# Optimization experiments

Measured on AMD Instinct MI355X. Metric: run time of the kernel, lower is better.

## Reference

```python
import jax, jax.numpy as jnp
import numpy as np

N = 256        # nagents
HID = 256      # hid_size
OBS = 128      # obs_size
GAT_HID = 128  # gat_hid_size
H1 = 4         # gat_num_heads (first processor)
H2 = 1         # gat_num_heads_out (second processor)
NACT = 10      # single action head
NEG = 0.2      # leaky relu negative slope


def _lin(k, fan_in, fan_out, s=0.05):
    kw, kb = jax.random.split(k)
    return (jax.random.normal(kw, (fan_in, fan_out), jnp.float32) * s,
            jax.random.normal(kb, (fan_out,), jnp.float32) * s)


def setup_inputs() -> dict:
    key = jax.random.key(0)
    ks = jax.random.split(key, 32)
    p = {}
    p['obs'] = jax.random.normal(ks[0], (1, N, OBS), jnp.float32)
    p['hidden_state'] = jax.random.normal(ks[1], (N, HID), jnp.float32)
    p['cell_state'] = jax.random.normal(ks[2], (N, HID), jnp.float32)
    p['w_obs'], p['b_obs'] = _lin(ks[3], OBS, HID)
    p['w_ih'], p['b_ih'] = _lin(ks[4], HID, 4 * HID)   # LSTMCell input->gates (i,f,g,o)
    p['w_hh'], p['b_hh'] = _lin(ks[5], HID, 4 * HID)
    p['w_me'], p['b_me'] = _lin(ks[6], HID, HID)        # message encoder
    p['w_md'], p['b_md'] = _lin(ks[7], HID, HID)        # message decoder
    # sub_scheduler_mlp1: 2*HID -> HID//2 -> HID//8 -> 2
    p['s1_w1'], p['s1_b1'] = _lin(ks[8], 2 * HID, HID // 2)
    p['s1_w2'], p['s1_b2'] = _lin(ks[9], HID // 2, HID // 8)
    p['s1_w3'], p['s1_b3'] = _lin(ks[10], HID // 8, 2)
    # sub_scheduler_mlp2 (learn_second_graph)
    p['s2_w1'], p['s2_b1'] = _lin(ks[11], 2 * HID, HID // 2)
    p['s2_w2'], p['s2_b2'] = _lin(ks[12], HID // 2, HID // 8)
    p['s2_w3'], p['s2_b3'] = _lin(ks[13], HID // 8, 2)
    # GAT1: HID -> H1*GAT_HID (concat heads)
    p['g1_w'] = jax.random.normal(ks[14], (HID, H1 * GAT_HID), jnp.float32) * 0.05
    p['g1_ai'] = jax.random.normal(ks[15], (H1, GAT_HID), jnp.float32) * 0.05
    p['g1_aj'] = jax.random.normal(ks[16], (H1, GAT_HID), jnp.float32) * 0.05
    p['g1_b'] = jax.random.normal(ks[17], (H1 * GAT_HID,), jnp.float32) * 0.05
    # GAT2: H1*GAT_HID -> HID (average over heads)
    p['g2_w'] = jax.random.normal(ks[18], (H1 * GAT_HID, H2 * HID), jnp.float32) * 0.05
    p['g2_ai'] = jax.random.normal(ks[19], (H2, HID), jnp.float32) * 0.05
    p['g2_aj'] = jax.random.normal(ks[20], (H2, HID), jnp.float32) * 0.05
    p['g2_b'] = jax.random.normal(ks[21], (HID,), jnp.float32) * 0.05
    p['w_v'], p['b_v'] = _lin(ks[22], 2 * HID, 1)
    p['w_a'], p['b_a'] = _lin(ks[23], 2 * HID, NACT)
    return p


def _sub_scheduler(h, w1, b1, w2, b2, w3, b3, mask, key):
    # pairwise concat: pair[i,j] = [h_i, h_j]  -> [n, n, 2*hid]
    n, d = h.shape
    pair = jnp.concatenate([jnp.broadcast_to(h[:, None, :], (n, n, d)),
                            jnp.broadcast_to(h[None, :, :], (n, n, d))], axis=-1)
    z = jax.nn.relu(pair @ w1 + b1)
    z = jax.nn.relu(z @ w2 + b2)
    logits = z @ w3 + b3                                # [n, n, 2]
    # gumbel-softmax (tau=1, hard=True, straight-through)
    u = jax.random.uniform(key, logits.shape, minval=1e-10, maxval=1.0)
    gumbel = -jnp.log(-jnp.log(u))
    y = jax.nn.softmax(logits + gumbel, axis=-1)
    y_hard = jax.nn.one_hot(jnp.argmax(y, axis=-1), 2, dtype=y.dtype)
    y = y_hard + y - jax.lax.stop_gradient(y)
    adj = y[..., 1] * mask * mask.T                     # mask [n,1]
    return adj


def _gat(x, adj, W, ai, aj, b, average):
    # dense-adjacency multi-head GAT, self_loop_type=1 (force self loops)
    n = x.shape[0]
    heads, of = ai.shape
    h = (x @ W).reshape(n, heads, of)                   # [n, heads, out]
    eye = jnp.eye(n, dtype=x.dtype)
    adj = adj * (1.0 - eye) + eye
    ci = jnp.einsum('nhf,hf->nh', h, ai)
    cj = jnp.einsum('nhf,hf->nh', h, aj)
    e = jax.nn.leaky_relu(ci[:, None, :] + cj[None, :, :], NEG)   # [n, n, heads]
    att = jnp.where(adj[:, :, None] > 0, e, jnp.float32(-9e15))
    att = jax.nn.softmax(att, axis=1)
    att = att * adj[:, :, None]
    out = jnp.einsum('ijh,jhf->ihf', att, h)            # aggregate over neighbors j
    out = out.mean(axis=1) if average else out.reshape(n, heads * of)
    return out + b


def reference(obs, hidden_state, cell_state, w_obs, b_obs, w_ih, b_ih, w_hh, b_hh,
              w_me, b_me, w_md, b_md,
              s1_w1, s1_b1, s1_w2, s1_b2, s1_w3, s1_b3,
              s2_w1, s2_b1, s2_w2, s2_b2, s2_w3, s2_b3,
              g1_w, g1_ai, g1_aj, g1_b, g2_w, g2_ai, g2_aj, g2_b,
              w_v, b_v, w_a, b_a):
    x = (obs @ w_obs + b_obs)[0]                        # [n, hid]
    # LSTMCell, torch gate order (i, f, g, o)
    gates = x @ w_ih + b_ih + hidden_state @ w_hh + b_hh
    i, f, g, o = jnp.split(gates, 4, axis=-1)
    c_new = jax.nn.sigmoid(f) * cell_state + jax.nn.sigmoid(i) * jnp.tanh(g)
    h_new = jax.nn.sigmoid(o) * jnp.tanh(c_new)
    mask = jnp.ones((N, 1), jnp.float32)                # all agents alive
    comm = (h_new @ w_me + b_me) * mask
    comm_ori = comm
    adj1 = _sub_scheduler(comm, s1_w1, s1_b1, s1_w2, s1_b2, s1_w3, s1_b3,
                          mask, jax.random.key(1))
    comm = jax.nn.elu(_gat(comm, adj1, g1_w, g1_ai, g1_aj, g1_b, average=False))
    adj2 = _sub_scheduler(comm_ori, s2_w1, s2_b1, s2_w2, s2_b2, s2_w3, s2_b3,
                          mask, jax.random.key(2))
    comm = _gat(comm, adj2, g2_w, g2_ai, g2_aj, g2_b, average=True)
    comm = (comm * mask) @ w_md + b_md
    value = jnp.concatenate([h_new, comm], axis=-1) @ w_v + b_v      # [n, 1]
    hc = jnp.concatenate([h_new.reshape(1, N, HID), comm.reshape(1, N, HID)], axis=-1)
    action_out = jax.nn.log_softmax(hc @ w_a + b_a, axis=-1)         # [1, n, nact]
    return action_out, value, h_new, c_new
```

## Files before the change

### kernel.cpp

```cpp
#include <hip/hip_runtime.h>
#include <stdint.h>
#include <math.h>

#define NA 256

typedef __attribute__((ext_vector_type(4))) float f32x4;
typedef __attribute__((ext_vector_type(8))) short bfrag;
typedef __attribute__((ext_vector_type(4))) float cfrag;

__device__ __forceinline__ uint32_t rotl32_(uint32_t v, int d) {
    return (v << d) | (v >> (32 - d));
}

__device__ uint32_t jax_random_bits(uint32_t key_lo, uint32_t flat) {
    uint32_t a, b;
    bool first;
    if (flat < 65536u) { a = flat; b = flat + 65536u; first = true; }
    else               { a = flat - 65536u; b = flat; first = false; }
    uint32_t ks0 = 0u, ks1 = key_lo, ks2 = 0u ^ key_lo ^ 0x1BD11BDAu;
    uint32_t x0 = a + ks0, x1 = b + ks1;
    const int r0[4] = {13, 15, 26, 6};
    const int r1[4] = {17, 29, 16, 24};
#define TF_R4(RS) { for (int rr = 0; rr < 4; ++rr) { x0 += x1; x1 = rotl32_(x1, RS[rr]); x1 ^= x0; } }
    TF_R4(r0); x0 += ks1; x1 += ks2 + 1u;
    TF_R4(r1); x0 += ks2; x1 += ks0 + 2u;
    TF_R4(r0); x0 += ks0; x1 += ks1 + 3u;
    TF_R4(r1); x0 += ks1; x1 += ks2 + 4u;
    TF_R4(r0); x0 += ks2; x1 += ks0 + 5u;
#undef TF_R4
    return first ? x0 : x1;
}

__device__ float jax_gumbel(uint32_t key_lo, uint32_t flat) {
    uint32_t bits = jax_random_bits(key_lo, flat);
    uint32_t v = (bits >> 9) | 0x3F800000u;
    float u = __uint_as_float(v) - 1.0f;
    u = u + 1e-10f;
    u = fmaxf(1e-10f, u);
    return -logf(-logf(u));
}

__device__ __forceinline__ uint32_t f2bf(float f) {
    uint32_t u = __float_as_uint(f);
    return (u + 0x7FFFu + ((u >> 16) & 1u)) >> 16;
}

__global__ __launch_bounds__(256) void k_lstm(
        const float* __restrict__ obs, const float* __restrict__ hs,
        const float* __restrict__ cs,
        const float* __restrict__ w_obs, const float* __restrict__ b_obs,
        const float* __restrict__ w_ih, const float* __restrict__ b_ih,
        const float* __restrict__ w_hh, const float* __restrict__ b_hh,
        float* __restrict__ h_out, float* __restrict__ c_out) {
    __shared__ float o_l[8][128];
    __shared__ float h_l[8][256];
    __shared__ float x_l[8][256];
    __shared__ float red[8192];
    int r0 = blockIdx.x * 8, c0 = blockIdx.y * 32, t = threadIdx.x;
    ((f32x4*)o_l)[t] = ((const f32x4*)(obs + r0 * 128))[t];
    ((f32x4*)h_l)[t] = ((const f32x4*)(hs + r0 * 256))[t];
    ((f32x4*)h_l)[t + 256] = ((const f32x4*)(hs + r0 * 256))[t + 256];
    __syncthreads();
    {
        int ks = t >> 6, q = t & 63;
        f32x4 acc[8];
#pragma unroll
        for (int r = 0; r < 8; ++r) acc[r] = (f32x4){0.f, 0.f, 0.f, 0.f};
#pragma unroll
        for (int k = ks * 32; k < ks * 32 + 32; ++k) {
            f32x4 w = *(const f32x4*)(w_obs + k * 256 + q * 4);
#pragma unroll
            for (int r = 0; r < 8; ++r) {
                float xv = o_l[r][k];
                acc[r].x += xv * w.x; acc[r].y += xv * w.y;
                acc[r].z += xv * w.z; acc[r].w += xv * w.w;
            }
        }
#pragma unroll
        for (int r = 0; r < 8; ++r)
            *(f32x4*)&red[(ks * 8 + r) * 256 + q * 4] = acc[r];
    }
    __syncthreads();
    {
#pragma unroll
        for (int rep = 0; rep < 8; ++rep) {
            int o = t + rep * 256;
            int r = o >> 8, c = o & 255;
            float s = b_obs[c];
#pragma unroll
            for (int k2 = 0; k2 < 4; ++k2) s += red[(k2 * 8 + r) * 256 + c];
            x_l[r][c] = s;
        }
    }
    __syncthreads();
    {
        int ks = t >> 5, cg = t & 31;
        int g = cg >> 3, qd = cg & 7;
        int col = g * 256 + c0 + qd * 4;
        const float* W = (ks < 4) ? w_ih : w_hh;
        const float* xl = (ks < 4) ? &x_l[0][0] : &h_l[0][0];
        int kb = (ks & 3) * 64;
        f32x4 acc[8];
#pragma unroll
        for (int r = 0; r < 8; ++r) acc[r] = (f32x4){0.f, 0.f, 0.f, 0.f};
#pragma unroll
        for (int kk = 0; kk < 64; ++kk) {
            int k = kb + kk;
            f32x4 w = *(const f32x4*)(W + k * 1024 + col);
#pragma unroll
            for (int r = 0; r < 8; ++r) {
                float xv = xl[r * 256 + k];
                acc[r].x += xv * w.x; acc[r].y += xv * w.y;
                acc[r].z += xv * w.z; acc[r].w += xv * w.w;
            }
        }
        __syncthreads();
#pragma unroll
        for (int r = 0; r < 8; ++r)
            *(f32x4*)&red[(ks * 8 + r) * 128 + cg * 4] = acc[r];
    }
    __syncthreads();
    {
        int r = t >> 5, hc = t & 31;
        int gc = c0 + hc;
        float gate[4];
#pragma unroll
        for (int g = 0; g < 4; ++g) {
            float s = b_ih[g * 256 + gc] + b_hh[g * 256 + gc];
#pragma unroll
            for (int ks = 0; ks < 8; ++ks) s += red[(ks * 8 + r) * 128 + g * 32 + hc];
            gate[g] = s;
        }
        float ig = 1.f / (1.f + expf(-gate[0]));
        float fg = 1.f / (1.f + expf(-gate[1]));
        float gg = tanhf(gate[2]);
        float og = 1.f / (1.f + expf(-gate[3]));
        float cn = fg * cs[(r0 + r) * 256 + gc] + ig * gg;
        float hn = og * tanhf(cn);
        h_out[(r0 + r) * 256 + gc] = hn;
        c_out[(r0 + r) * 256 + gc] = cn;
    }
}

template<int K>
__device__ __forceinline__ void gemm_core(const float* __restrict__ X, int xs, int r0,
                                          const float* __restrict__ W, int ws,
                                          const float* __restrict__ bias,
                                          float* __restrict__ Y, int ys, int t,
                                          float* xr, float* red) {
    constexpr int KQ = K / 4;
#pragma unroll
    for (int q = t; q < 2 * K; q += 256) {
        int r = q / KQ, c = q % KQ;
        ((f32x4*)xr)[r * KQ + c] = ((const f32x4*)(X + (r0 + r) * xs))[c];
    }
    __syncthreads();
    constexpr int KP = K / 16;
    int qd = t & 15, ks = t >> 4;
    f32x4 acc[8];
#pragma unroll
    for (int r = 0; r < 8; ++r) acc[r] = (f32x4){0.f, 0.f, 0.f, 0.f};
#pragma unroll
    for (int k = ks * KP; k < ks * KP + KP; ++k) {
        f32x4 w = *(const f32x4*)(W + k * ws + qd * 4);
#pragma unroll
        for (int r = 0; r < 8; ++r) {
            float xv = xr[r * K + k];
            acc[r].x += xv * w.x; acc[r].y += xv * w.y;
            acc[r].z += xv * w.z; acc[r].w += xv * w.w;
        }
    }
#pragma unroll
    for (int r = 0; r < 8; ++r)
        *(f32x4*)&red[(ks * 8 + r) * 64 + qd * 4] = acc[r];
    __syncthreads();
#pragma unroll
    for (int rep = 0; rep < 2; ++rep) {
        int o = t + rep * 256;
        int r = o >> 6, c = o & 63;
        float s = bias ? bias[c] : 0.f;
#pragma unroll
        for (int ks2 = 0; ks2 < 16; ++ks2) s += red[(ks2 * 8 + r) * 64 + c];
        Y[(r0 + r) * ys + c] = s;
    }
}

template<int K>
__global__ __launch_bounds__(256) void k_gemm(const float* __restrict__ X, int xs,
                                              const float* __restrict__ W, int ws,
                                              const float* __restrict__ bias,
                                              float* __restrict__ Y, int ys) {
    __shared__ float xr[8 * K];
    __shared__ float red[16 * 8 * 64];
    int cb = blockIdx.y * 64;
    gemm_core<K>(X, xs, blockIdx.x * 8, W + cb, ws, bias ? bias + cb : nullptr,
                 Y + cb, ys, threadIdx.x, xr, red);
}

__global__ __launch_bounds__(256) void k_mgemm(const float* __restrict__ comm,
        const float* __restrict__ g1_w,
        const float* __restrict__ s1w1, const float* __restrict__ s1b1,
        const float* __restrict__ s2w1, const float* __restrict__ s2b1,
        float* __restrict__ h1, float* __restrict__ A1, float* __restrict__ B1,
        float* __restrict__ A2, float* __restrict__ B2) {
    __shared__ float xr[8 * 256];
    __shared__ float red[16 * 8 * 64];
    int y = blockIdx.y;
    const float* W; int ws; const float* bias; float* Y; int ys;
    if (y < 8) {
        W = g1_w + y * 64; ws = 512; bias = nullptr; Y = h1 + y * 64; ys = 512;
    } else {
        int idx = y - 8;
        int sel = idx >> 2, part = (idx >> 1) & 1, half = idx & 1;
        W = (sel ? s2w1 : s1w1) + part * (256 * 128) + half * 64; ws = 128;
        bias = part ? nullptr : ((sel ? s2b1 : s1b1) + half * 64);
        float* tgt = sel ? (part ? B2 : A2) : (part ? B1 : A1);
        Y = tgt + half * 64; ys = 128;
    }
    gemm_core<256>(comm, 256, blockIdx.x * 8, W, ws, bias, Y, ys, threadIdx.x, xr, red);
}

__global__ __launch_bounds__(256) void k_sched(
        const float* __restrict__ A1, const float* __restrict__ B1,
        const float* __restrict__ s1w2, const float* __restrict__ s1b2,
        const float* __restrict__ s1w3, const float* __restrict__ s1b3,
        const float* __restrict__ A2, const float* __restrict__ B2,
        const float* __restrict__ s2w2, const float* __restrict__ s2b2,
        const float* __restrict__ s2w3, const float* __restrict__ s2b3,
        float* __restrict__ adj1, float* __restrict__ adj2) {
    __shared__ __align__(16) char z1z2[65536];
    __shared__ __align__(16) char w2l[8192];
    __shared__ float a_l[128];
    __shared__ float b2_l[32], w3_l[64], b3_l[2];
    int i = blockIdx.x, t = threadIdx.x, s = blockIdx.y;
    const float* A  = s ? A2 : A1;
    const float* B  = s ? B2 : B1;
    const float* w2 = s ? s2w2 : s1w2;
    const float* b2 = s ? s2b2 : s1b2;
    const float* w3 = s ? s2w3 : s1w3;
    const float* b3 = s ? s2b3 : s1b3;
    float* adj = s ? adj2 : adj1;
    uint32_t key_lo = (uint32_t)(s + 1);

    if (t < 32) ((f32x4*)a_l)[t] = ((const f32x4*)(A + i * 128))[t];
    if (t < 32) b2_l[t] = b2[t];
    if (t < 64) w3_l[t] = w3[t];
    if (t < 2)  b3_l[t] = b3[t];
    {
        int c = t & 31, kq = t >> 5;
        uint32_t* dst = (uint32_t*)w2l;
#pragma unroll
        for (int e = 0; e < 8; ++e) {
            int k = kq * 16 + e * 2;
            uint32_t word = f2bf(w2[k * 32 + c]) | (f2bf(w2[(k + 1) * 32 + c]) << 16);
            int byte = (c * 256 + k * 2) ^ ((c & 7) << 4);
            dst[byte >> 2] = word;
        }
    }
    __syncthreads();
#pragma unroll
    for (int rep = 0; rep < 4; ++rep) {
        int j = (t >> 2) + rep * 64;
        int kq = t & 3;
        const f32x4* bp = (const f32x4*)(B + j * 128 + kq * 32);
        uint32_t words[16];
#pragma unroll
        for (int q = 0; q < 8; ++q) {
            f32x4 bv = bp[q];
            int k = kq * 32 + q * 4;
            float z0 = fmaxf(a_l[k] + bv.x, 0.f);
            float z1v = fmaxf(a_l[k + 1] + bv.y, 0.f);
            float z2v = fmaxf(a_l[k + 2] + bv.z, 0.f);
            float z3v = fmaxf(a_l[k + 3] + bv.w, 0.f);
            words[q * 2]     = f2bf(z0) | (f2bf(z1v) << 16);
            words[q * 2 + 1] = f2bf(z2v) | (f2bf(z3v) << 16);
        }
#pragma unroll
        for (int w4 = 0; w4 < 4; ++w4) {
            int byte = (j * 256 + kq * 64 + w4 * 16) ^ ((j & 7) << 4);
            *(uint4*)(z1z2 + byte) = make_uint4(words[w4 * 4], words[w4 * 4 + 1],
                                                words[w4 * 4 + 2], words[w4 * 4 + 3]);
        }
    }
    __syncthreads();
    int w = t >> 6, l = t & 63;
    bfrag bf[2][4];
#pragma unroll
    for (int ct = 0; ct < 2; ++ct)
#pragma unroll
        for (int ks = 0; ks < 4; ++ks) {
            int col = ct * 16 + (l & 15);
            int k = ks * 32 + (l >> 4) * 8;
            int byte = (col * 256 + k * 2) ^ ((col & 7) << 4);
            bf[ct][ks] = *(bfrag*)(w2l + byte);
        }
    cfrag acc[4][2];
    cfrag zz = {0.f, 0.f, 0.f, 0.f};
#pragma unroll
    for (int rt = 0; rt < 4; ++rt) { acc[rt][0] = zz; acc[rt][1] = zz; }
#pragma unroll
    for (int rt = 0; rt < 4; ++rt) {
        int j = (w * 4 + rt) * 16 + (l & 15);
#pragma unroll
        for (int ks = 0; ks < 4; ++ks) {
            int byte = (j * 256 + (ks * 32 + (l >> 4) * 8) * 2) ^ ((j & 7) << 4);
            bfrag af = *(bfrag*)(z1z2 + byte);
            acc[rt][0] = __builtin_amdgcn_mfma_f32_16x16x32_bf16(af, bf[0][ks], acc[rt][0], 0, 0, 0);
            acc[rt][1] = __builtin_amdgcn_mfma_f32_16x16x32_bf16(af, bf[1][ks], acc[rt][1], 0, 0, 0);
        }
    }
    __syncthreads();
    float* z2 = (float*)z1z2;
#pragma unroll
    for (int rt = 0; rt < 4; ++rt)
#pragma unroll
        for (int ct = 0; ct < 2; ++ct)
#pragma unroll
            for (int r = 0; r < 4; ++r) {
                int j = (w * 4 + rt) * 16 + (l >> 4) * 4 + r;
                int c = ct * 16 + (l & 15);
                z2[j * 36 + c] = acc[rt][ct][r];
            }
    __syncthreads();
    {
        int j = t;
        float p0 = 0.f, p1 = 0.f;
#pragma unroll
        for (int c = 0; c < 32; ++c) {
            float zv = fmaxf(z2[j * 36 + c] + b2_l[c], 0.f);
            p0 += zv * w3_l[2 * c];
            p1 += zv * w3_l[2 * c + 1];
        }
        float l0 = p0 + b3_l[0], l1 = p1 + b3_l[1];
        uint32_t flat = (uint32_t)(i * 256 + j) * 2u;
        float g0 = jax_gumbel(key_lo, flat);
        float g1 = jax_gumbel(key_lo, flat + 1u);
        adj[i * 256 + j] = (l1 + g1 > l0 + g0) ? 1.0f : 0.0f;
    }
}

__global__ void k_attc(const float* __restrict__ H, const float* __restrict__ ai,
                       const float* __restrict__ aj, float* __restrict__ ci,
                       float* __restrict__ cj, int heads, int F) {
    int n = blockIdx.x, lane = threadIdx.x;
    for (int h = 0; h < heads; ++h) {
        float pi = 0.f, pj = 0.f;
        for (int f = lane; f < F; f += 64) {
            float v = H[n * heads * F + h * F + f];
            pi += v * ai[h * F + f];
            pj += v * aj[h * F + f];
        }
        for (int off = 32; off; off >>= 1) {
            pi += __shfl_xor(pi, off);
            pj += __shfl_xor(pj, off);
        }
        if (lane == 0) { ci[n * heads + h] = pi; cj[n * heads + h] = pj; }
    }
}

__global__ __launch_bounds__(256) void k_gat1(const float* __restrict__ H,
        const float* __restrict__ adj, const float* __restrict__ ci,
        const float* __restrict__ cj, const float* __restrict__ bias,
        float* __restrict__ out) {
    __shared__ float att[2][4][256];
    __shared__ float red[4][2][256];
    int i0 = blockIdx.x * 2, cb = blockIdx.y * 256, t = threadIdx.x;
#pragma unroll
    for (int r = 0; r < 2; ++r) {
        int i = i0 + r;
        float adjv = (t == i) ? 1.f : adj[i * 256 + t];
#pragma unroll
        for (int h = 0; h < 4; ++h) {
            float e = ci[i * 4 + h] + cj[t * 4 + h];
            e = e >= 0.f ? e : 0.2f * e;
            att[r][h][t] = adjv > 0.f ? e : -INFINITY;
        }
    }
    __syncthreads();
    {
        int wv = t >> 6, lane = t & 63;
        for (int p = wv; p < 8; p += 4) {
            int r = p >> 2, h = p & 3;
            float* ar = att[r][h];
            float m = -INFINITY;
            for (int j = lane; j < 256; j += 64) m = fmaxf(m, ar[j]);
            for (int off = 32; off; off >>= 1) m = fmaxf(m, __shfl_xor(m, off));
            float vals[4], sm = 0.f;
#pragma unroll
            for (int q = 0; q < 4; ++q) {
                float v = expf(ar[lane + 64 * q] - m);
                vals[q] = v; sm += v;
            }
            for (int off = 32; off; off >>= 1) sm += __shfl_xor(sm, off);
            float inv = 1.f / sm;
#pragma unroll
            for (int q = 0; q < 4; ++q) ar[lane + 64 * q] = vals[q] * inv;
        }
    }
    __syncthreads();
    {
        int q = t & 63, js = t >> 6;
        int c = cb + q * 4;
        int h = c >> 7;
        f32x4 a0 = {0.f, 0.f, 0.f, 0.f}, a1 = a0;
        const float* ar0 = att[0][h];
        const float* ar1 = att[1][h];
#pragma unroll
        for (int j = js * 64; j < js * 64 + 64; ++j) {
            f32x4 hv = *(const f32x4*)(H + j * 512 + c);
            float v0 = ar0[j], v1 = ar1[j];
            a0.x += v0 * hv.x; a0.y += v0 * hv.y; a0.z += v0 * hv.z; a0.w += v0 * hv.w;
            a1.x += v1 * hv.x; a1.y += v1 * hv.y; a1.z += v1 * hv.z; a1.w += v1 * hv.w;
        }
        *(f32x4*)&red[js][0][q * 4] = a0;
        *(f32x4*)&red[js][1][q * 4] = a1;
    }
    __syncthreads();
#pragma unroll
    for (int rep = 0; rep < 2; ++rep) {
        int o = t + rep * 256;
        int r = o >> 8, c = o & 255;
        float s = red[0][r][c] + red[1][r][c] + red[2][r][c] + red[3][r][c] + bias[cb + c];
        out[(i0 + r) * 512 + cb + c] = s > 0.f ? s : expm1f(s);
    }
}

__global__ __launch_bounds__(256) void k_final(const float* __restrict__ H,
        const float* __restrict__ adj, const float* __restrict__ ci,
        const float* __restrict__ cj, const float* __restrict__ g2_b,
        const float* __restrict__ w_md, const float* __restrict__ b_md,
        const float* __restrict__ h_new,
        const float* __restrict__ w_v, const float* __restrict__ b_v,
        const float* __restrict__ w_a, const float* __restrict__ b_a,
        float* __restrict__ value, float* __restrict__ action) {
    __shared__ float att[256];
    __shared__ float buf[4][256];
    __shared__ float out2[256];
    __shared__ float comm3[256];
    __shared__ float hrow[256];
    __shared__ float hred[4][16];
    __shared__ float vred[4];
    int i = blockIdx.x, t = threadIdx.x;
    hrow[t] = h_new[i * 256 + t];
    {
        float adjv = (t == i) ? 1.f : adj[i * 256 + t];
        float e = ci[i] + cj[t];
        e = e >= 0.f ? e : 0.2f * e;
        att[t] = adjv > 0.f ? e : -INFINITY;
    }
    __syncthreads();
    {
        int lane = t & 63;
        float m = -INFINITY;
        for (int j = lane; j < 256; j += 64) m = fmaxf(m, att[j]);
        for (int off = 32; off; off >>= 1) m = fmaxf(m, __shfl_xor(m, off));
        float sm = 0.f;
        for (int j = lane; j < 256; j += 64) sm += expf(att[j] - m);
        for (int off = 32; off; off >>= 1) sm += __shfl_xor(sm, off);
        float inv = 1.f / sm;
        float myval = expf(att[t] - m) * inv;
        __syncthreads();
        att[t] = myval;
    }
    __syncthreads();
    {
        int q = t & 63, js = t >> 6;
        f32x4 acc = {0.f, 0.f, 0.f, 0.f};
#pragma unroll
        for (int j = js * 64; j < js * 64 + 64; ++j) {
            f32x4 hv = *(const f32x4*)(H + j * 256 + q * 4);
            float av = att[j];
            acc.x += av * hv.x; acc.y += av * hv.y; acc.z += av * hv.z; acc.w += av * hv.w;
        }
        *(f32x4*)&buf[js][q * 4] = acc;
    }
    __syncthreads();
    out2[t] = buf[0][t] + buf[1][t] + buf[2][t] + buf[3][t] + g2_b[t];
    __syncthreads();
    {
        int q = t & 63, ks = t >> 6;
        f32x4 acc = {0.f, 0.f, 0.f, 0.f};
#pragma unroll
        for (int k = ks * 64; k < ks * 64 + 64; ++k) {
            f32x4 wv = *(const f32x4*)(w_md + k * 256 + q * 4);
            float xv = out2[k];
            acc.x += xv * wv.x; acc.y += xv * wv.y; acc.z += xv * wv.z; acc.w += xv * wv.w;
        }
        *(f32x4*)&buf[ks][q * 4] = acc;
    }
    __syncthreads();
    comm3[t] = buf[0][t] + buf[1][t] + buf[2][t] + buf[3][t] + b_md[t];
    __syncthreads();
    int w = t >> 6, l = t & 63;
    {
        float p = hrow[t] * w_v[t] + comm3[t] * w_v[256 + t];
        for (int off = 32; off; off >>= 1) p += __shfl_xor(p, off);
        if (l == 0) vred[w] = p;
    }
    {
        int o = l & 15;
        int kseg = w * 4 + (l >> 4);
        float acc = 0.f;
        if (o < 10) {
#pragma unroll
            for (int kk = 0; kk < 32; ++kk) {
                int k = kseg * 32 + kk;
                float x = (kseg < 8) ? hrow[k] : comm3[k - 256];
                acc += x * w_a[k * 10 + o];
            }
        }
        acc += __shfl_xor(acc, 16);
        acc += __shfl_xor(acc, 32);
        if (l < 16) hred[w][l] = acc;
    }
    __syncthreads();
    if (t < 16) {
        int o = t;
        float logit = (o < 10)
            ? hred[0][o] + hred[1][o] + hred[2][o] + hred[3][o] + b_a[o]
            : -INFINITY;
        float m = logit;
        for (int off = 8; off; off >>= 1) m = fmaxf(m, __shfl_xor(m, off));
        float ex = (o < 10) ? expf(logit - m) : 0.f;
        float sm = ex;
        for (int off = 8; off; off >>= 1) sm += __shfl_xor(sm, off);
        if (o < 10) action[i * 10 + o] = logit - m - logf(sm);
        if (o == 0) value[i] = vred[0] + vred[1] + vred[2] + vred[3] + b_v[0];
    }
}

extern "C" void kernel_launch(void* const* d_in, const int* in_sizes, int n_in,
                              void* d_out, int out_size, void* d_ws, size_t ws_size,
                              hipStream_t stream) {
    const float* obs   = (const float*)d_in[0];
    const float* hs    = (const float*)d_in[1];
    const float* cs    = (const float*)d_in[2];
    const float* w_obs = (const float*)d_in[3];
    const float* b_obs = (const float*)d_in[4];
    const float* w_ih  = (const float*)d_in[5];
    const float* b_ih  = (const float*)d_in[6];
    const float* w_hh  = (const float*)d_in[7];
    const float* b_hh  = (const float*)d_in[8];
    const float* w_me  = (const float*)d_in[9];
    const float* b_me  = (const float*)d_in[10];
    const float* w_md  = (const float*)d_in[11];
    const float* b_md  = (const float*)d_in[12];
    const float* s1_w1 = (const float*)d_in[13];
    const float* s1_b1 = (const float*)d_in[14];
    const float* s1_w2 = (const float*)d_in[15];
    const float* s1_b2 = (const float*)d_in[16];
    const float* s1_w3 = (const float*)d_in[17];
    const float* s1_b3 = (const float*)d_in[18];
    const float* s2_w1 = (const float*)d_in[19];
    const float* s2_b1 = (const float*)d_in[20];
    const float* s2_w2 = (const float*)d_in[21];
    const float* s2_b2 = (const float*)d_in[22];
    const float* s2_w3 = (const float*)d_in[23];
    const float* s2_b3 = (const float*)d_in[24];
    const float* g1_w  = (const float*)d_in[25];
    const float* g1_ai = (const float*)d_in[26];
    const float* g1_aj = (const float*)d_in[27];
    const float* g1_b  = (const float*)d_in[28];
    const float* g2_w  = (const float*)d_in[29];
    const float* g2_ai = (const float*)d_in[30];
    const float* g2_aj = (const float*)d_in[31];
    const float* g2_b  = (const float*)d_in[32];
    const float* w_v   = (const float*)d_in[33];
    const float* b_v   = (const float*)d_in[34];
    const float* w_a   = (const float*)d_in[35];
    const float* b_a   = (const float*)d_in[36];

    float* out = (float*)d_out;
    float* action = out;
    float* value  = out + 2560;
    float* h_new  = out + 2816;
    float* c_new  = out + 68352;

    float* ws = (float*)d_ws;
    float* comm  = ws;
    float* A1    = ws + 65536;
    float* B1    = ws + 98304;
    float* A2    = ws + 131072;
    float* B2    = ws + 163840;
    float* adj1  = ws + 196608;
    float* adj2  = ws + 262144;
    float* h1    = ws + 327680;
    float* ci1   = ws + 458752;
    float* cj1   = ws + 459776;
    float* comm2 = ws + 460800;
    float* h2    = ws + 591872;
    float* ci2   = ws + 657408;
    float* cj2   = ws + 657664;

    k_lstm<<<dim3(32, 8), 256, 0, stream>>>(obs, hs, cs, w_obs, b_obs,
                                            w_ih, b_ih, w_hh, b_hh, h_new, c_new);
    k_gemm<256><<<dim3(32, 4), 256, 0, stream>>>(h_new, 256, w_me, 256, b_me, comm, 256);
    k_mgemm<<<dim3(32, 16), 256, 0, stream>>>(comm, g1_w, s1_w1, s1_b1, s2_w1, s2_b1,
                                              h1, A1, B1, A2, B2);
    k_sched<<<dim3(256, 2), 256, 0, stream>>>(A1, B1, s1_w2, s1_b2, s1_w3, s1_b3,
                                              A2, B2, s2_w2, s2_b2, s2_w3, s2_b3,
                                              adj1, adj2);
    k_attc<<<NA, 64, 0, stream>>>(h1, g1_ai, g1_aj, ci1, cj1, 4, 128);
    k_gat1<<<dim3(128, 2), 256, 0, stream>>>(h1, adj1, ci1, cj1, g1_b, comm2);
    k_gemm<512><<<dim3(32, 4), 256, 0, stream>>>(comm2, 512, g2_w, 256, nullptr, h2, 256);
    k_attc<<<NA, 64, 0, stream>>>(h2, g2_ai, g2_aj, ci2, cj2, 1, 256);
    k_final<<<NA, 256, 0, stream>>>(h2, adj2, ci2, cj2, g2_b, w_md, b_md, h_new,
                                    w_v, b_v, w_a, b_a, value, action);
}
```

Measured before the change: 73.71 us.

## Fuse GAT attention coefficient dot-products into preceding GEMM epilogues

```diff
diff --git a/kernel.cpp b/kernel.cpp
--- a/kernel.cpp
+++ b/kernel.cpp
@@ -51,12 +51,18 @@
         const float* __restrict__ w_obs, const float* __restrict__ b_obs,
         const float* __restrict__ w_ih, const float* __restrict__ b_ih,
         const float* __restrict__ w_hh, const float* __restrict__ b_hh,
-        float* __restrict__ h_out, float* __restrict__ c_out) {
+        float* __restrict__ h_out, float* __restrict__ c_out,
+        float* __restrict__ ci1, float* __restrict__ cj1,
+        float* __restrict__ ci2, float* __restrict__ cj2) {
     __shared__ float o_l[8][128];
     __shared__ float h_l[8][256];
     __shared__ float x_l[8][256];
     __shared__ float red[8192];
     int r0 = blockIdx.x * 8, c0 = blockIdx.y * 32, t = threadIdx.x;
+    if (blockIdx.x == 0 && blockIdx.y == 0) {
+        for (int idx = t; idx < 1024; idx += 256) { ci1[idx] = 0.f; cj1[idx] = 0.f; }
+        ci2[t] = 0.f; cj2[t] = 0.f;
+    }
     ((f32x4*)o_l)[t] = ((const f32x4*)(obs + r0 * 128))[t];
     ((f32x4*)h_l)[t] = ((const f32x4*)(hs + r0 * 256))[t];
     ((f32x4*)h_l)[t + 256] = ((const f32x4*)(hs + r0 * 256))[t + 256];
@@ -81,16 +87,14 @@
             *(f32x4*)&red[(ks * 8 + r) * 256 + q * 4] = acc[r];
     }
     __syncthreads();
-    {
-#pragma unroll
-        for (int rep = 0; rep < 8; ++rep) {
-            int o = t + rep * 256;
-            int r = o >> 8, c = o & 255;
-            float s = b_obs[c];
-#pragma unroll
-            for (int k2 = 0; k2 < 4; ++k2) s += red[(k2 * 8 + r) * 256 + c];
-            x_l[r][c] = s;
-        }
+#pragma unroll
+    for (int rep = 0; rep < 8; ++rep) {
+        int o = t + rep * 256;
+        int r = o >> 8, c = o & 255;
+        float s = b_obs[c];
+#pragma unroll
+        for (int k2 = 0; k2 < 4; ++k2) s += red[(k2 * 8 + r) * 256 + c];
+        x_l[r][c] = s;
     }
     __syncthreads();
     {
@@ -198,14 +202,16 @@
 }
 
 __global__ __launch_bounds__(256) void k_mgemm(const float* __restrict__ comm,
-        const float* __restrict__ g1_w,
+        const float* __restrict__ g1_w, const float* __restrict__ g1ai,
+        const float* __restrict__ g1aj,
         const float* __restrict__ s1w1, const float* __restrict__ s1b1,
         const float* __restrict__ s2w1, const float* __restrict__ s2b1,
         float* __restrict__ h1, float* __restrict__ A1, float* __restrict__ B1,
-        float* __restrict__ A2, float* __restrict__ B2) {
+        float* __restrict__ A2, float* __restrict__ B2,
+        float* __restrict__ ci1, float* __restrict__ cj1) {
     __shared__ float xr[8 * 256];
     __shared__ float red[16 * 8 * 64];
-    int y = blockIdx.y;
+    int y = blockIdx.y, t = threadIdx.x, r0 = blockIdx.x * 8;
     const float* W; int ws; const float* bias; float* Y; int ys;
     if (y < 8) {
         W = g1_w + y * 64; ws = 512; bias = nullptr; Y = h1 + y * 64; ys = 512;
@@ -217,7 +223,54 @@
         float* tgt = sel ? (part ? B2 : A2) : (part ? B1 : A1);
         Y = tgt + half * 64; ys = 128;
     }
-    gemm_core<256>(comm, 256, blockIdx.x * 8, W, ws, bias, Y, ys, threadIdx.x, xr, red);
+#pragma unroll
+    for (int q = t; q < 512; q += 256) {
+        int r = q >> 6, c = q & 63;
+        ((f32x4*)xr)[r * 64 + c] = ((const f32x4*)(comm + (r0 + r) * 256))[c];
+    }
+    __syncthreads();
+    int qd = t & 15, ks = t >> 4;
+    f32x4 acc[8];
+#pragma unroll
+    for (int r = 0; r < 8; ++r) acc[r] = (f32x4){0.f, 0.f, 0.f, 0.f};
+#pragma unroll
+    for (int k = ks * 16; k < ks * 16 + 16; ++k) {
+        f32x4 w = *(const f32x4*)(W + k * ws + qd * 4);
+#pragma unroll
+        for (int r = 0; r < 8; ++r) {
+            float xv = xr[r * 256 + k];
+            acc[r].x += xv * w.x; acc[r].y += xv * w.y;
+            acc[r].z += xv * w.z; acc[r].w += xv * w.w;
+        }
+    }
+#pragma unroll
+    for (int r = 0; r < 8; ++r)
+        *(f32x4*)&red[(ks * 8 + r) * 64 + qd * 4] = acc[r];
+    __syncthreads();
+#pragma unroll
+    for (int rep = 0; rep < 2; ++rep) {
+        int o = t + rep * 256;
+        int r = o >> 6, c = o & 63;
+        float s = bias ? bias[c] : 0.f;
+#pragma unroll
+        for (int ks2 = 0; ks2 < 16; ++ks2) s += red[(ks2 * 8 + r) * 64 + c];
+        Y[(r0 + r) * ys + c] = s;
+        if (y < 8) {
+            int h = y >> 1;
+            int f = ((y & 1) << 6) + c;
+            float pi = s * g1ai[h * 128 + f];
+            float pj = s * g1aj[h * 128 + f];
+#pragma unroll
+            for (int off = 32; off; off >>= 1) {
+                pi += __shfl_xor(pi, off);
+                pj += __shfl_xor(pj, off);
+            }
+            if ((t & 63) == 0) {
+                atomicAdd(&ci1[(r0 + r) * 4 + h], pi);
+                atomicAdd(&cj1[(r0 + r) * 4 + h], pj);
+            }
+        }
+    }
 }
 
 __global__ __launch_bounds__(256) void k_sched(
@@ -339,25 +392,6 @@
     }
 }
 
-__global__ void k_attc(const float* __restrict__ H, const float* __restrict__ ai,
-                       const float* __restrict__ aj, float* __restrict__ ci,
-                       float* __restrict__ cj, int heads, int F) {
-    int n = blockIdx.x, lane = threadIdx.x;
-    for (int h = 0; h < heads; ++h) {
-        float pi = 0.f, pj = 0.f;
-        for (int f = lane; f < F; f += 64) {
-            float v = H[n * heads * F + h * F + f];
-            pi += v * ai[h * F + f];
-            pj += v * aj[h * F + f];
-        }
-        for (int off = 32; off; off >>= 1) {
-            pi += __shfl_xor(pi, off);
-            pj += __shfl_xor(pj, off);
-        }
-        if (lane == 0) { ci[n * heads + h] = pi; cj[n * heads + h] = pj; }
-    }
-}
-
 __global__ __launch_bounds__(256) void k_gat1(const float* __restrict__ H,
         const float* __restrict__ adj, const float* __restrict__ ci,
         const float* __restrict__ cj, const float* __restrict__ bias,
@@ -422,6 +456,60 @@
         int r = o >> 8, c = o & 255;
         float s = red[0][r][c] + red[1][r][c] + red[2][r][c] + red[3][r][c] + bias[cb + c];
         out[(i0 + r) * 512 + cb + c] = s > 0.f ? s : expm1f(s);
+    }
+}
+
+__global__ __launch_bounds__(256) void k_g2gemm(const float* __restrict__ comm2,
+        const float* __restrict__ g2w, const float* __restrict__ g2ai,
+        const float* __restrict__ g2aj, float* __restrict__ h2,
+        float* __restrict__ ci2, float* __restrict__ cj2) {
+    __shared__ float xr[8 * 512];
+    __shared__ float red[16 * 8 * 64];
+    int t = threadIdx.x, r0 = blockIdx.x * 8, cb = blockIdx.y * 64;
+    const float* W = g2w + cb;
+#pragma unroll
+    for (int q = t; q < 1024; q += 256) {
+        int r = q >> 7, c = q & 127;
+        ((f32x4*)xr)[r * 128 + c] = ((const f32x4*)(comm2 + (r0 + r) * 512))[c];
+    }
+    __syncthreads();
+    int qd = t & 15, ks = t >> 4;
+    f32x4 acc[8];
+#pragma unroll
+    for (int r = 0; r < 8; ++r) acc[r] = (f32x4){0.f, 0.f, 0.f, 0.f};
+#pragma unroll
+    for (int k = ks * 32; k < ks * 32 + 32; ++k) {
+        f32x4 w = *(const f32x4*)(W + k * 256 + qd * 4);
+#pragma unroll
+        for (int r = 0; r < 8; ++r) {
+            float xv = xr[r * 512 + k];
+            acc[r].x += xv * w.x; acc[r].y += xv * w.y;
+            acc[r].z += xv * w.z; acc[r].w += xv * w.w;
+        }
+    }
+#pragma unroll
+    for (int r = 0; r < 8; ++r)
+        *(f32x4*)&red[(ks * 8 + r) * 64 + qd * 4] = acc[r];
+    __syncthreads();
+#pragma unroll
+    for (int rep = 0; rep < 2; ++rep) {
+        int o = t + rep * 256;
+        int r = o >> 6, c = o & 63;
+        float s = 0.f;
+#pragma unroll
+        for (int ks2 = 0; ks2 < 16; ++ks2) s += red[(ks2 * 8 + r) * 64 + c];
+        h2[(r0 + r) * 256 + cb + c] = s;
+        float pi = s * g2ai[cb + c];
+        float pj = s * g2aj[cb + c];
+#pragma unroll
+        for (int off = 32; off; off >>= 1) {
+            pi += __shfl_xor(pi, off);
+            pj += __shfl_xor(pj, off);
+        }
+        if ((t & 63) == 0) {
+            atomicAdd(&ci2[r0 + r], pi);
+            atomicAdd(&cj2[r0 + r], pj);
+        }
     }
 }
 
@@ -593,17 +681,17 @@
     float* cj2   = ws + 657664;
 
     k_lstm<<<dim3(32, 8), 256, 0, stream>>>(obs, hs, cs, w_obs, b_obs,
-                                            w_ih, b_ih, w_hh, b_hh, h_new, c_new);
+                                            w_ih, b_ih, w_hh, b_hh, h_new, c_new,
+                                            ci1, cj1, ci2, cj2);
     k_gemm<256><<<dim3(32, 4), 256, 0, stream>>>(h_new, 256, w_me, 256, b_me, comm, 256);
-    k_mgemm<<<dim3(32, 16), 256, 0, stream>>>(comm, g1_w, s1_w1, s1_b1, s2_w1, s2_b1,
-                                              h1, A1, B1, A2, B2);
+    k_mgemm<<<dim3(32, 16), 256, 0, stream>>>(comm, g1_w, g1_ai, g1_aj,
+                                              s1_w1, s1_b1, s2_w1, s2_b1,
+                                              h1, A1, B1, A2, B2, ci1, cj1);
     k_sched<<<dim3(256, 2), 256, 0, stream>>>(A1, B1, s1_w2, s1_b2, s1_w3, s1_b3,
                                               A2, B2, s2_w2, s2_b2, s2_w3, s2_b3,
                                               adj1, adj2);
-    k_attc<<<NA, 64, 0, stream>>>(h1, g1_ai, g1_aj, ci1, cj1, 4, 128);
     k_gat1<<<dim3(128, 2), 256, 0, stream>>>(h1, adj1, ci1, cj1, g1_b, comm2);
-    k_gemm<512><<<dim3(32, 4), 256, 0, stream>>>(comm2, 512, g2_w, 256, nullptr, h2, 256);
-    k_attc<<<NA, 64, 0, stream>>>(h2, g2_ai, g2_aj, ci2, cj2, 1, 256);
+    k_g2gemm<<<dim3(32, 4), 256, 0, stream>>>(comm2, g2_w, g2_ai, g2_aj, h2, ci2, cj2);
     k_final<<<NA, 256, 0, stream>>>(h2, adj2, ci2, cj2, g2_b, w_md, b_md, h_new,
                                     w_v, b_v, w_a, b_a, value, action);
 }
```

Result: faster. 69.32 us (-6.0%).
